# Optimization experiments

Measured on AMD Instinct MI355X. Metric: run time of the kernel, lower is better.

The kernel has to match this reference:

```python
import jax, jax.numpy as jnp
import numpy as np

B, S, P, H, W, TAG, M, K = 4, 2, 17, 128, 128, 1, 8, 10
PHW = P * H * W
SIGMA, SF = 0.2, 3.0
E_INV = float(np.e ** -1)
EPS = 1e-6


def setup_inputs() -> dict:
    key = jax.random.key(0)
    k1, k2, k3, k4, k5, k6, k7 = jax.random.split(key, 7)
    preds = jax.random.normal(k1, (B, S, (1 + TAG) * P, H, W), jnp.float32)
    gt_masks = jax.random.uniform(k2, (B, H, W), jnp.float32)
    gt_heatmaps = jax.random.uniform(k3, (B, P, H, W), jnp.float32)
    pos = jax.random.uniform(k4, (B, M, P, 2), jnp.float32) * H  # pixel coords
    vis = jax.random.randint(k5, (B, M, P, 1), 0, 2).astype(jnp.float32)
    gt_skeletons = jnp.concatenate([pos, vis], axis=-1)  # [B,M,P,3] = (x, y, vis)
    kp_idx = jax.random.randint(k6, (B, M, P, 1), 0, PHW)
    kp_vis = jax.random.randint(k7, (B, M, P, 1), 0, 2)
    gt_keypoints = jnp.concatenate([kp_idx, kp_vis], axis=-1).astype(jnp.int32)  # [B,M,J,2]
    return {"preds": preds, "gt_masks": gt_masks, "gt_heatmaps": gt_heatmaps,
            "gt_skeletons": gt_skeletons, "gt_keypoints": gt_keypoints}


def _clog(x):
    # torch BCE clamps log at -100
    return jnp.clip(jnp.log(x), -100.0, None)


def _tag_single(pt, kp):
    # pt: [TAG, PHW] tag map for one (image, stack); kp: [M, J, 2] int (flat_idx, vis)
    idx = kp[..., 0]
    vis = (kp[..., 1] > 0).astype(pt.dtype)  # [M, J]
    g = jnp.transpose(pt[:, idx], (1, 2, 0))  # [M, J, TAG]
    cnt = vis.sum(1)  # [M]
    valid = (cnt > 0).astype(pt.dtype)
    safe = jnp.maximum(cnt, 1.0)
    mean_tag = (g * vis[..., None]).sum(1) / safe[:, None]  # [M, TAG]
    # pull: per-person mean over (visible joints x tag dims) of squared deviation
    pull_pp = (((g - mean_tag[:, None]) ** 2) * vis[..., None]).sum((1, 2)) / (safe * TAG)
    num = valid.sum()
    pull = (pull_pp * valid).sum() / (num + EPS)
    d = ((mean_tag[:, None] - mean_tag[None]) ** 2).sum(-1)  # [M, M]
    pm = jnp.exp(-d) * valid[:, None] * valid[None]
    push = (pm.sum() - num) / ((num - 1.0) * num + EPS) * 0.5
    return push, pull


def _forward(preds, gt_masks, gt_heatmaps, gt_skeletons, gt_keypoints):
    hm = preds[:, :, :P]  # [B,S,P,H,W] raw heatmap logits
    prob = jax.nn.sigmoid(hm)
    # ---- detection loss (weighted BCE, per stack) ----
    t = (gt_heatmaps > E_INV).astype(jnp.float32)[:, None]  # [B,1,P,H,W]
    wgt = 10.0 * t + 0.5 * (gt_heatmaps < E_INV).astype(jnp.float32)[:, None]
    x = prob * gt_masks[:, None, None]
    bce = -(t * _clog(x) + (1.0 - t) * _clog(1.0 - x))
    det_loss = (wgt * bce).mean(axis=(0, 2, 3, 4))  # [S]
    # ---- associative embedding push/pull ----
    pred_tag_imgs = preds[:, :, P:(1 + TAG) * P].reshape(B, S, TAG, P, H, W)
    pred_tags = pred_tag_imgs.reshape(B, S, TAG, PHW)
    push, pull = jax.vmap(lambda ptb, kpb: jax.vmap(lambda pt: _tag_single(pt, kpb))(ptb))(
        pred_tags, gt_keypoints)  # each [B,S]
    # ---- keypoint sampling: top-K of flattened probability maps ----
    flat = prob.reshape(B, S, PHW)
    _, topi = jax.lax.top_k(flat, K)  # [B,S,K]
    part = topi // (H * W)
    rem = topi % (H * W)
    xi = rem // W
    yi = rem % W
    pos = jnp.stack([xi, yi], -1).astype(jnp.float32)  # [B,S,K,2]
    # ---- nearest-person matching (faithful to source, incl. vis==1 penalty) ----
    max_dist = float(H + W)
    sk_t = jnp.transpose(gt_skeletons, (0, 2, 1, 3))  # [B,P,M,3]
    pidx = jnp.broadcast_to(part.reshape(B, S * K)[:, :, None, None], (B, S * K, M, 3))
    sk_sel = jnp.take_along_axis(sk_t, pidx, axis=1).reshape(B, S, K, M, 3)
    vispen = max_dist * (sk_sel[..., 2] == 1).astype(jnp.float32)  # [B,S,K,M]
    dvec = vispen[..., None] + sk_sel[..., 1:] - pos[..., None, :]
    dist = jnp.sqrt((dvec ** 2).sum(-1) + 1e-12)
    person_ids = jnp.argmin(dist, axis=-1)  # [B,S,K]
    # ---- gather tag values at sampled locations ----
    pti = jnp.transpose(pred_tag_imgs, (0, 1, 3, 4, 5, 2))  # [B,S,P,H,W,TAG]
    bb = jnp.arange(B)[:, None, None]
    ss = jnp.arange(S)[None, :, None]
    tv = pti[bb, ss, part, xi, yi]  # [B,S,K,TAG]
    # ---- SkeletonGenerator: tag-conditioned soft-argmax ----
    aff = ((pti[:, :, None] - tv[:, :, :, None, None, None, :]) ** 2).sum(-1)  # [B,S,K,P,H,W]
    logits = SF * hm[:, :, None] - aff / (2.0 * SIGMA ** 2)
    wts = jax.nn.softmax(logits.reshape(B, S, K, P, H * W), -1).reshape(B, S, K, P, H, W)
    px = (wts * jnp.arange(H, dtype=jnp.float32)[:, None]).sum((-1, -2))  # [B,S,K,P]
    py = (wts * jnp.arange(W, dtype=jnp.float32)).sum((-1, -2))
    skel = jnp.stack([px, py], -1)  # [B,S,K,P,2]
    gts = gt_skeletons[bb, person_ids]  # [B,S,K,P,3]
    err = jnp.sqrt(((gts[..., :2] - skel) ** 2).sum(-1) + 1e-12) * (gts[..., 2] > 0)
    delta = 0.1
    a = jnp.abs(err)
    small = (a < delta).astype(jnp.float32)
    hub = small * err ** 2 + (1.0 - small) * delta * (a - delta / 2.0)
    skel_loss = hub.mean(-1).mean(-1)  # [B,S]
    # ---- weighted sum (loss_weights = (1,1,1,10)) ----
    return (1.0 * push.mean() + 1.0 * pull.mean() + 1.0 * det_loss.mean()
            + 10.0 * skel_loss.mean())


def reference(preds, gt_masks, gt_heatmaps, gt_skeletons, gt_keypoints):
    return _forward(preds, gt_masks, gt_heatmaps, gt_skeletons, gt_keypoints)
```

## Files before the change

### kernel.cpp

```cpp
#include <hip/hip_runtime.h>
#include <math.h>

#define B_ 4
#define S_ 2
#define P_ 17
#define H_ 128
#define W_ 128
#define M_ 8
#define K_ 10
#define HW_ (H_*W_)
#define PHW_ (P_*HW_)
#define CH_ 34
#define G_ 68
#define C_ 4096
#define E_INV_F 0.36787944117144233f
#define LOG2E 1.4426950408889634f
#define SF_ 3.0f
#define INV2SIG 12.5f
#define MAXDIST 256.0f

#define MAIN_BLOCKS (B_*S_*G_)
#define SKEL_CHUNKS 4
#define NBSP (B_*S_*P_)
#define SKEL_BLOCKS (NBSP*SKEL_CHUNKS)

__device__ __forceinline__ unsigned int map32(float f) {
    unsigned int u = __float_as_uint(f);
    unsigned int flip = (unsigned int)((int)u >> 31) | 0x80000000u;
    return u ^ flip;
}

__device__ __forceinline__ void insert10(unsigned long long* a, unsigned long long key) {
    bool c[10];
    #pragma unroll
    for (int j = 0; j < 10; ++j) c[j] = key > a[j];
    #pragma unroll
    for (int j = 9; j >= 1; --j)
        a[j] = c[j-1] ? a[j-1] : (c[j] ? key : a[j]);
    a[0] = c[0] ? key : a[0];
}

__device__ __forceinline__ void merge10(unsigned long long* a, const unsigned long long* b) {
    #pragma unroll
    for (int t = 0; t < 10; ++t) {
        unsigned long long key = b[t];
        if (key > a[9]) insert10(a, key);
    }
}

__global__ __launch_bounds__(256) void k_main(const float* __restrict__ preds,
                                              const float* __restrict__ gmask,
                                              const float* __restrict__ gh,
                                              unsigned long long* __restrict__ cand,
                                              float* __restrict__ ws_det) {
    int bs = blockIdx.x / G_;
    int c  = blockIdx.x % G_;
    int p    = c >> 2;
    int quarter = c & 3;
    int b    = bs / S_;
    int tid  = threadIdx.x;
    const float4* base = (const float4*)preds + (size_t)bs*CH_*4096 + (size_t)c*1024;
    const float4* gm4p = (const float4*)gmask + (size_t)b*4096 + quarter*1024;
    const float4* gh4p = (const float4*)gh + ((size_t)b*P_ + p)*4096 + quarter*1024;

    unsigned long long a[10];
    #pragma unroll
    for (int j = 0; j < 10; ++j) a[j] = 0ull;
    float det_acc = 0.0f;

    #pragma unroll
    for (int j = 0; j < 4; ++j) {
        int q = j*256 + tid;
        float4 hv = base[q];
        float4 gm = gm4p[q];
        float4 gv = gh4p[q];
        unsigned int i0 = (unsigned int)(c*C_ + q*4);
        const float* hvv = &hv.x; const float* gmv = &gm.x; const float* ghv4 = &gv.x;
        #pragma unroll
        for (int cc = 0; cc < 4; ++cc) {
            float hm = hvv[cc];
            unsigned long long key =
                ((unsigned long long)map32(hm) << 32) | (unsigned int)(~(i0 + cc));
            insert10(a, key);
            float e = exp2f(-fabsf(hm)*LOG2E);
            float r = __builtin_amdgcn_rcpf(1.0f + e);
            float prob = (hm >= 0.0f) ? r : e*r;
            float x = prob * gmv[cc];
            float ghv = ghv4[cc];
            float tt  = (ghv > E_INV_F) ? 1.0f : 0.0f;
            float wgt = 10.0f*tt + ((ghv < E_INV_F) ? 0.5f : 0.0f);
            float lx  = fmaxf(__logf(x),        -100.0f);
            float l1x = fmaxf(__logf(1.0f - x), -100.0f);
            det_acc += wgt * (-(tt*lx + (1.0f - tt)*l1x));
        }
    }
    #pragma unroll
    for (int off = 32; off > 0; off >>= 1) det_acc += __shfl_down(det_acc, off);
    __shared__ float sred[4];
    int wave = tid >> 6, lane = tid & 63;
    if (lane == 0) sred[wave] = det_acc;
    __shared__ unsigned long long sm[256*10];
    #pragma unroll
    for (int j = 0; j < 10; ++j) sm[tid*10+j] = a[j];
    __syncthreads();
    if (tid == 0) ws_det[blockIdx.x] = sred[0] + sred[1] + sred[2] + sred[3];
    for (int st = 128; st >= 1; st >>= 1) {
        if (tid < st) {
            unsigned long long x[10], y[10];
            #pragma unroll
            for (int j = 0; j < 10; ++j) { x[j] = sm[tid*10+j]; y[j] = sm[(tid+st)*10+j]; }
            merge10(x, y);
            #pragma unroll
            for (int j = 0; j < 10; ++j) sm[tid*10+j] = x[j];
        }
        __syncthreads();
    }
    if (tid < 10) cand[(size_t)blockIdx.x*10 + tid] = sm[tid];
}

__global__ __launch_bounds__(256) void k_tt(const float* __restrict__ preds,
                                            const float* __restrict__ gsk,
                                            const int* __restrict__ kp,
                                            const unsigned long long* __restrict__ cand,
                                            float* __restrict__ ws_tag,
                                            float* __restrict__ ws_tv,
                                            int* __restrict__ ws_pid) {
    int bs = blockIdx.x; int b = bs / S_;
    int tid = threadIdx.x;
    const float* tagbase = preds + ((size_t)bs*CH_ + P_)*HW_;
    __shared__ float g[M_*P_];
    __shared__ float vis[M_*P_];
    __shared__ float mean_tag[M_];
    __shared__ float validm[M_];
    __shared__ float pull_pp[M_];
    if (tid < M_*P_) {
        int m = tid / P_; int pp = tid % P_;
        int off = ((b*M_ + m)*P_ + pp)*2;
        int idx = kp[off];
        int v   = kp[off+1];
        g[tid]   = tagbase[idx];
        vis[tid] = (v > 0) ? 1.0f : 0.0f;
    }
    __syncthreads();
    if (tid < M_) {
        float cnt = 0.0f, sum = 0.0f;
        for (int pp = 0; pp < P_; pp++) { cnt += vis[tid*P_+pp]; sum += g[tid*P_+pp]*vis[tid*P_+pp]; }
        float safe = fmaxf(cnt, 1.0f);
        float mt = sum / safe;
        mean_tag[tid] = mt;
        validm[tid] = (cnt > 0.0f) ? 1.0f : 0.0f;
        float pl = 0.0f;
        for (int pp = 0; pp < P_; pp++) { float d = g[tid*P_+pp] - mt; pl += d*d*vis[tid*P_+pp]; }
        pull_pp[tid] = pl / safe;
    }
    __syncthreads();
    if (tid == 0) {
        float num = 0.0f;
        for (int m = 0; m < M_; m++) num += validm[m];
        float pull = 0.0f;
        for (int m = 0; m < M_; m++) pull += pull_pp[m]*validm[m];
        pull = pull / (num + 1e-6f);
        float pmsum = 0.0f;
        for (int i = 0; i < M_; i++)
            for (int j = 0; j < M_; j++) {
                float d = mean_tag[i] - mean_tag[j]; d = d*d;
                pmsum += expf(-d)*validm[i]*validm[j];
            }
        float push = (pmsum - num) / ((num - 1.0f)*num + 1e-6f) * 0.5f;
        ws_tag[bs] = push + pull;
    }
    __shared__ unsigned long long sm[128*10];
    if (tid < 128) {
        if (tid < G_) {
            #pragma unroll
            for (int j = 0; j < 10; ++j) sm[tid*10+j] = cand[((size_t)bs*G_ + tid)*10 + j];
        } else {
            #pragma unroll
            for (int j = 0; j < 10; ++j) sm[tid*10+j] = 0ull;
        }
    }
    __syncthreads();
    for (int st = 64; st >= 1; st >>= 1) {
        if (tid < st) {
            unsigned long long x[10], y[10];
            #pragma unroll
            for (int j = 0; j < 10; ++j) { x[j] = sm[tid*10+j]; y[j] = sm[(tid+st)*10+j]; }
            merge10(x, y);
            #pragma unroll
            for (int j = 0; j < 10; ++j) sm[tid*10+j] = x[j];
        }
        __syncthreads();
    }
    if (tid < K_) {
        unsigned long long key = sm[tid];
        unsigned int topi = (unsigned int)(~key);
        int part = topi >> 14;
        int rem  = topi & (HW_-1);
        int xi   = rem >> 7;
        int yi   = rem & (W_-1);
        float tv = tagbase[topi];
        float best = INFINITY; int pid = 0;
        for (int m = 0; m < M_; m++) {
            const float* sk = gsk + ((size_t)(b*M_ + m)*P_ + part)*3;
            float sk1 = sk[1], sk2 = sk[2];
            float vp = (sk2 == 1.0f) ? MAXDIST : 0.0f;
            float d0 = vp + sk1 - (float)xi;
            float d1 = vp + sk2 - (float)yi;
            float dist = sqrtf(d0*d0 + d1*d1 + 1e-12f);
            if (dist < best) { best = dist; pid = m; }
        }
        int o = bs*K_ + tid;
        ws_tv[o]  = tv;
        ws_pid[o] = pid;
    }
}

__global__ __launch_bounds__(256) void k_skel(const float* __restrict__ preds,
                                              const float* __restrict__ ws_tv,
                                              float* __restrict__ ws_skl,
                                              float* __restrict__ ws_ssx,
                                              float* __restrict__ ws_ssy) {
    int bid   = blockIdx.x / SKEL_CHUNKS;
    int chunk = blockIdx.x % SKEL_CHUNKS;
    int p  = bid % P_;
    int bs = bid / P_;
    const float4* hm4 = (const float4*)(preds + ((size_t)bs*CH_ + p)*HW_);
    const float4* tg4 = (const float4*)(preds + ((size_t)bs*CH_ + P_ + p)*HW_);
    float tv[K_];
    #pragma unroll
    for (int k = 0; k < K_; k++) tv[k] = ws_tv[bs*K_ + k];
    float l[K_], sx[K_], sy[K_];
    #pragma unroll
    for (int k = 0; k < K_; k++) { l[k] = 0.0f; sx[k] = 0.0f; sy[k] = 0.0f; }
    int tid = threadIdx.x;
    const float C2 = INV2SIG * LOG2E;
    #pragma unroll
    for (int j = 0; j < 4; ++j) {
        int q = chunk*1024 + j*256 + tid;
        float4 hv = hm4[q];
        float4 tg = tg4[q];
        float h  = (float)(q >> 5);
        float w0 = (float)((q*4) & (W_-1));
        const float* hvv = &hv.x; const float* tgv = &tg.x;
        #pragma unroll
        for (int cc = 0; cc < 4; ++cc) {
            float a2 = (SF_*LOG2E) * hvv[cc];
            float tgc = tgv[cc];
            float w = w0 + (float)cc;
            #pragma unroll
            for (int k = 0; k < K_; k++) {
                float d = tgc - tv[k];
                float e = exp2f(fmaf(-C2, d*d, a2));
                l[k] += e;
                sx[k] = fmaf(e, h, sx[k]);
                sy[k] = fmaf(e, w, sy[k]);
            }
        }
    }
    #pragma unroll
    for (int k = 0; k < K_; k++) {
        for (int off = 32; off > 0; off >>= 1) {
            l[k]  += __shfl_down(l[k],  off);
            sx[k] += __shfl_down(sx[k], off);
            sy[k] += __shfl_down(sy[k], off);
        }
    }
    __shared__ float red[4][K_][3];
    int wave = tid >> 6, lane = tid & 63;
    if (lane == 0) {
        #pragma unroll
        for (int k = 0; k < K_; k++) {
            red[wave][k][0] = l[k]; red[wave][k][1] = sx[k]; red[wave][k][2] = sy[k];
        }
    }
    __syncthreads();
    if (tid < K_) {
        int k = tid;
        float L  = red[0][k][0] + red[1][k][0] + red[2][k][0] + red[3][k][0];
        float SX = red[0][k][1] + red[1][k][1] + red[2][k][1] + red[3][k][1];
        float SY = red[0][k][2] + red[1][k][2] + red[2][k][2] + red[3][k][2];
        int o = blockIdx.x*K_ + k;
        ws_skl[o] = L; ws_ssx[o] = SX; ws_ssy[o] = SY;
    }
}

__global__ __launch_bounds__(256) void k_fin(const float* __restrict__ gsk,
                                             const int* __restrict__ ws_pid,
                                             const float* __restrict__ ws_skl,
                                             const float* __restrict__ ws_ssx,
                                             const float* __restrict__ ws_ssy,
                                             const float* __restrict__ ws_det,
                                             const float* __restrict__ ws_tag,
                                             float* __restrict__ out) {
    int tid = threadIdx.x;
    float acc = 0.0f;
    for (int i = tid; i < MAIN_BLOCKS; i += 256) acc += ws_det[i];
    acc *= (1.0f/(float)(B_*S_*P_*HW_));
    if (tid < B_*S_) acc += ws_tag[tid] * (1.0f/(float)(B_*S_));
    for (int idx = tid; idx < NBSP*K_; idx += 256) {
        int bid = idx / K_;
        int k   = idx % K_;
        int p  = bid % P_;
        int bs = bid / P_;
        int b  = bs / S_;
        float L = 0.0f, SX = 0.0f, SY = 0.0f;
        #pragma unroll
        for (int c = 0; c < SKEL_CHUNKS; ++c) {
            int o = (bid*SKEL_CHUNKS + c)*K_ + k;
            L += ws_skl[o]; SX += ws_ssx[o]; SY += ws_ssy[o];
        }
        float px = SX / L, py = SY / L;
        int pid = ws_pid[bs*K_ + k];
        const float* g = gsk + ((size_t)(b*M_ + pid)*P_ + p)*3;
        float d0 = g[0] - px, d1 = g[1] - py;
        float gate = (g[2] > 0.0f) ? 1.0f : 0.0f;
        float err = sqrtf(d0*d0 + d1*d1 + 1e-12f) * gate;
        float hub = (err < 0.1f) ? err*err : 0.1f*(err - 0.05f);
        acc += hub * (10.0f/(float)(B_*S_*K_*P_));
    }
    #pragma unroll
    for (int off = 32; off > 0; off >>= 1) acc += __shfl_down(acc, off);
    __shared__ float sred[4];
    int wave = tid >> 6, lane = tid & 63;
    if (lane == 0) sred[wave] = acc;
    __syncthreads();
    if (tid == 0) out[0] = sred[0] + sred[1] + sred[2] + sred[3];
}

extern "C" void kernel_launch(void* const* d_in, const int* in_sizes, int n_in,
                              void* d_out, int out_size, void* d_ws, size_t ws_size,
                              hipStream_t stream) {
    (void)in_sizes; (void)n_in; (void)out_size; (void)ws_size;
    const float* preds = (const float*)d_in[0];
    const float* gmask = (const float*)d_in[1];
    const float* gh    = (const float*)d_in[2];
    const float* gsk   = (const float*)d_in[3];
    const int*   gkp   = (const int*)d_in[4];
    float* out = (float*)d_out;
    unsigned long long* cand = (unsigned long long*)d_ws;
    float* ws_tv  = (float*)(cand + (size_t)MAIN_BLOCKS*10);
    int*   ws_pid = (int*)(ws_tv + (size_t)B_*S_*K_);
    float* ws_skl = (float*)(ws_pid + (size_t)B_*S_*K_);
    float* ws_ssx = ws_skl + (size_t)SKEL_BLOCKS*K_;
    float* ws_ssy = ws_ssx + (size_t)SKEL_BLOCKS*K_;
    float* ws_det = ws_ssy + (size_t)SKEL_BLOCKS*K_;
    float* ws_tag = ws_det + MAIN_BLOCKS;

    hipLaunchKernelGGL(k_main, dim3(MAIN_BLOCKS), dim3(256), 0, stream,
                       preds, gmask, gh, cand, ws_det);
    hipLaunchKernelGGL(k_tt,   dim3(B_*S_),       dim3(256), 0, stream,
                       preds, gsk, gkp, cand, ws_tag, ws_tv, ws_pid);
    hipLaunchKernelGGL(k_skel, dim3(SKEL_BLOCKS), dim3(256), 0, stream,
                       preds, ws_tv, ws_skl, ws_ssx, ws_ssy);
    hipLaunchKernelGGL(k_fin,  dim3(1),           dim3(256), 0, stream,
                       gsk, ws_pid, ws_skl, ws_ssx, ws_ssy, ws_det, ws_tag, out);
}
```

Measured before the change: 136.6 us.

## Fuse four kernels into one persistent kernel with atomic grid barriers

Merges the main detection/top-k pass, the tag/top-k merge, the skeleton softmax pass and the final reduction into one kernel launch of 544 blocks. Stages are ordered by atomic counters with spin-waits, and a last-block-done pattern performs the final reduction. The goal is to remove per-launch overhead and inter-kernel gaps. In exchange it relies on all blocks being co-resident to avoid deadlock, and it adds a memset launch plus spin-wait costs.

```diff
diff --git a/kernel.cpp b/kernel.cpp
--- a/kernel.cpp
+++ b/kernel.cpp
@@ -19,10 +19,9 @@
 #define INV2SIG 12.5f
 #define MAXDIST 256.0f
 
-#define MAIN_BLOCKS (B_*S_*G_)
+#define NBLK (B_*S_*G_)
 #define SKEL_CHUNKS 4
 #define NBSP (B_*S_*P_)
-#define SKEL_BLOCKS (NBSP*SKEL_CHUNKS)
 
 __device__ __forceinline__ unsigned int map32(float f) {
     unsigned int u = __float_as_uint(f);
@@ -48,283 +47,298 @@
     }
 }
 
-__global__ __launch_bounds__(256) void k_main(const float* __restrict__ preds,
-                                              const float* __restrict__ gmask,
-                                              const float* __restrict__ gh,
-                                              unsigned long long* __restrict__ cand,
-                                              float* __restrict__ ws_det) {
-    int bs = blockIdx.x / G_;
-    int c  = blockIdx.x % G_;
-    int p    = c >> 2;
-    int quarter = c & 3;
-    int b    = bs / S_;
-    int tid  = threadIdx.x;
-    const float4* base = (const float4*)preds + (size_t)bs*CH_*4096 + (size_t)c*1024;
-    const float4* gm4p = (const float4*)gmask + (size_t)b*4096 + quarter*1024;
-    const float4* gh4p = (const float4*)gh + ((size_t)b*P_ + p)*4096 + quarter*1024;
-
-    unsigned long long a[10];
-    #pragma unroll
-    for (int j = 0; j < 10; ++j) a[j] = 0ull;
-    float det_acc = 0.0f;
-
-    #pragma unroll
-    for (int j = 0; j < 4; ++j) {
-        int q = j*256 + tid;
-        float4 hv = base[q];
-        float4 gm = gm4p[q];
-        float4 gv = gh4p[q];
-        unsigned int i0 = (unsigned int)(c*C_ + q*4);
-        const float* hvv = &hv.x; const float* gmv = &gm.x; const float* ghv4 = &gv.x;
-        #pragma unroll
-        for (int cc = 0; cc < 4; ++cc) {
-            float hm = hvv[cc];
-            unsigned long long key =
-                ((unsigned long long)map32(hm) << 32) | (unsigned int)(~(i0 + cc));
-            insert10(a, key);
-            float e = exp2f(-fabsf(hm)*LOG2E);
-            float r = __builtin_amdgcn_rcpf(1.0f + e);
-            float prob = (hm >= 0.0f) ? r : e*r;
-            float x = prob * gmv[cc];
-            float ghv = ghv4[cc];
-            float tt  = (ghv > E_INV_F) ? 1.0f : 0.0f;
-            float wgt = 10.0f*tt + ((ghv < E_INV_F) ? 0.5f : 0.0f);
-            float lx  = fmaxf(__logf(x),        -100.0f);
-            float l1x = fmaxf(__logf(1.0f - x), -100.0f);
-            det_acc += wgt * (-(tt*lx + (1.0f - tt)*l1x));
-        }
-    }
-    #pragma unroll
-    for (int off = 32; off > 0; off >>= 1) det_acc += __shfl_down(det_acc, off);
+__device__ __forceinline__ void spin_until(unsigned int* p, unsigned int target) {
+    while (__hip_atomic_load(p, __ATOMIC_ACQUIRE, __HIP_MEMORY_SCOPE_AGENT) != target) {
+        __builtin_amdgcn_s_sleep(8);
+    }
+}
+
+#define BLOCK_RELEASE(CTR)  do { __syncthreads(); __threadfence(); __syncthreads(); \
+                                 if (tid == 0) atomicAdd((CTR), 1u); } while (0)
+
+__global__ __launch_bounds__(256, 3) void k_all(const float* __restrict__ preds,
+                                                const float* __restrict__ gmask,
+                                                const float* __restrict__ gh,
+                                                const float* __restrict__ gsk,
+                                                const int* __restrict__ kp,
+                                                unsigned int* __restrict__ ctr,
+                                                unsigned long long* __restrict__ cand,
+                                                float* __restrict__ ws_tv,
+                                                int* __restrict__ ws_pid,
+                                                float* __restrict__ ws_skl,
+                                                float* __restrict__ ws_ssx,
+                                                float* __restrict__ ws_ssy,
+                                                float* __restrict__ ws_det,
+                                                float* __restrict__ ws_tag,
+                                                float* __restrict__ out) {
+    int tid = threadIdx.x;
+    int blk = blockIdx.x;
+    int wave = tid >> 6, lane = tid & 63;
+
+    __shared__ unsigned long long sm[256*10];
+    __shared__ float s_g[M_*P_], s_vis[M_*P_];
+    __shared__ float s_mt[M_], s_val[M_], s_pp[M_];
     __shared__ float sred[4];
-    int wave = tid >> 6, lane = tid & 63;
-    if (lane == 0) sred[wave] = det_acc;
-    __shared__ unsigned long long sm[256*10];
-    #pragma unroll
-    for (int j = 0; j < 10; ++j) sm[tid*10+j] = a[j];
+    __shared__ float red[4][K_][3];
+    __shared__ int   s_last;
+
+    {
+        int bs = blk / G_;
+        int c  = blk % G_;
+        int p       = c >> 2;
+        int quarter = c & 3;
+        int b       = bs / S_;
+        const float4* base = (const float4*)preds + (size_t)bs*CH_*1024*4 + (size_t)c*1024;
+        const float4* gm4p = (const float4*)gmask + (size_t)b*4096 + quarter*1024;
+        const float4* gh4p = (const float4*)gh + ((size_t)b*P_ + p)*4096 + quarter*1024;
+
+        unsigned long long a[10];
+        #pragma unroll
+        for (int j = 0; j < 10; ++j) a[j] = 0ull;
+        float det_acc = 0.0f;
+
+        #pragma unroll
+        for (int j = 0; j < 4; ++j) {
+            int q = j*256 + tid;
+            float4 hv = base[q];
+            float4 gm = gm4p[q];
+            float4 gv = gh4p[q];
+            unsigned int i0 = (unsigned int)(c*C_ + q*4);
+            const float* hvv = &hv.x; const float* gmv = &gm.x; const float* ghv4 = &gv.x;
+            #pragma unroll
+            for (int cc = 0; cc < 4; ++cc) {
+                float hm = hvv[cc];
+                unsigned long long key =
+                    ((unsigned long long)map32(hm) << 32) | (unsigned int)(~(i0 + cc));
+                insert10(a, key);
+                float e = exp2f(-fabsf(hm)*LOG2E);
+                float r = __builtin_amdgcn_rcpf(1.0f + e);
+                float prob = (hm >= 0.0f) ? r : e*r;
+                float x = prob * gmv[cc];
+                float ghv = ghv4[cc];
+                float tt  = (ghv > E_INV_F) ? 1.0f : 0.0f;
+                float wgt = 10.0f*tt + ((ghv < E_INV_F) ? 0.5f : 0.0f);
+                float lx  = fmaxf(__logf(x),        -100.0f);
+                float l1x = fmaxf(__logf(1.0f - x), -100.0f);
+                det_acc += wgt * (-(tt*lx + (1.0f - tt)*l1x));
+            }
+        }
+        #pragma unroll
+        for (int off = 32; off > 0; off >>= 1) det_acc += __shfl_down(det_acc, off);
+        if (lane == 0) sred[wave] = det_acc;
+        #pragma unroll
+        for (int j = 0; j < 10; ++j) sm[tid*10+j] = a[j];
+        __syncthreads();
+        if (tid == 0) ws_det[blk] = sred[0] + sred[1] + sred[2] + sred[3];
+        for (int st = 128; st >= 1; st >>= 1) {
+            if (tid < st) {
+                unsigned long long x[10], y[10];
+                #pragma unroll
+                for (int j = 0; j < 10; ++j) { x[j] = sm[tid*10+j]; y[j] = sm[(tid+st)*10+j]; }
+                merge10(x, y);
+                #pragma unroll
+                for (int j = 0; j < 10; ++j) sm[tid*10+j] = x[j];
+            }
+            __syncthreads();
+        }
+        if (tid < 10) cand[(size_t)blk*10 + tid] = sm[tid];
+    }
+    if (blk < B_*S_) {
+        int bs2 = blk; int b2 = bs2 / S_;
+        const float* tagbase = preds + ((size_t)bs2*CH_ + P_)*HW_;
+        if (tid < M_*P_) {
+            int m = tid / P_; int pp = tid % P_;
+            int off = ((b2*M_ + m)*P_ + pp)*2;
+            s_g[tid]   = tagbase[kp[off]];
+            s_vis[tid] = (kp[off+1] > 0) ? 1.0f : 0.0f;
+        }
+        __syncthreads();
+        if (tid < M_) {
+            float cnt = 0.0f, sum = 0.0f;
+            for (int pp = 0; pp < P_; pp++) { cnt += s_vis[tid*P_+pp]; sum += s_g[tid*P_+pp]*s_vis[tid*P_+pp]; }
+            float safe = fmaxf(cnt, 1.0f);
+            float mt = sum / safe;
+            s_mt[tid] = mt;
+            s_val[tid] = (cnt > 0.0f) ? 1.0f : 0.0f;
+            float pl = 0.0f;
+            for (int pp = 0; pp < P_; pp++) { float d = s_g[tid*P_+pp] - mt; pl += d*d*s_vis[tid*P_+pp]; }
+            s_pp[tid] = pl / safe;
+        }
+        __syncthreads();
+        if (tid == 0) {
+            float num = 0.0f;
+            for (int m = 0; m < M_; m++) num += s_val[m];
+            float pull = 0.0f;
+            for (int m = 0; m < M_; m++) pull += s_pp[m]*s_val[m];
+            pull = pull / (num + 1e-6f);
+            float pmsum = 0.0f;
+            for (int i = 0; i < M_; i++)
+                for (int j = 0; j < M_; j++) {
+                    float d = s_mt[i] - s_mt[j]; d = d*d;
+                    pmsum += expf(-d)*s_val[i]*s_val[j];
+                }
+            float push = (pmsum - num) / ((num - 1.0f)*num + 1e-6f) * 0.5f;
+            ws_tag[bs2] = push + pull;
+        }
+    }
+    BLOCK_RELEASE(&ctr[0]);
+
+    if (blk < B_*S_) {
+        if (tid == 0) spin_until(&ctr[0], NBLK);
+        __syncthreads();
+        __threadfence();
+        int bs2 = blk; int b2 = bs2 / S_;
+        if (tid < 128) {
+            if (tid < G_) {
+                #pragma unroll
+                for (int j = 0; j < 10; ++j) sm[tid*10+j] = cand[((size_t)bs2*G_ + tid)*10 + j];
+            } else {
+                #pragma unroll
+                for (int j = 0; j < 10; ++j) sm[tid*10+j] = 0ull;
+            }
+        }
+        __syncthreads();
+        for (int st = 64; st >= 1; st >>= 1) {
+            if (tid < st) {
+                unsigned long long x[10], y[10];
+                #pragma unroll
+                for (int j = 0; j < 10; ++j) { x[j] = sm[tid*10+j]; y[j] = sm[(tid+st)*10+j]; }
+                merge10(x, y);
+                #pragma unroll
+                for (int j = 0; j < 10; ++j) sm[tid*10+j] = x[j];
+            }
+            __syncthreads();
+        }
+        if (tid < K_) {
+            unsigned long long key = sm[tid];
+            unsigned int topi = (unsigned int)(~key);
+            int part = topi >> 14;
+            int rem  = topi & (HW_-1);
+            int xi   = rem >> 7;
+            int yi   = rem & (W_-1);
+            const float* tagbase = preds + ((size_t)bs2*CH_ + P_)*HW_;
+            float tv = tagbase[topi];
+            float best = INFINITY; int pid = 0;
+            for (int m = 0; m < M_; m++) {
+                const float* sk = gsk + ((size_t)(b2*M_ + m)*P_ + part)*3;
+                float sk1 = sk[1], sk2 = sk[2];
+                float vp = (sk2 == 1.0f) ? MAXDIST : 0.0f;
+                float d0 = vp + sk1 - (float)xi;
+                float d1 = vp + sk2 - (float)yi;
+                float dist = sqrtf(d0*d0 + d1*d1 + 1e-12f);
+                if (dist < best) { best = dist; pid = m; }
+            }
+            ws_tv[bs2*K_ + tid]  = tv;
+            ws_pid[bs2*K_ + tid] = pid;
+        }
+        BLOCK_RELEASE(&ctr[8]);
+    }
+    if (tid == 0) spin_until(&ctr[8], (unsigned int)(B_*S_));
     __syncthreads();
-    if (tid == 0) ws_det[blockIdx.x] = sred[0] + sred[1] + sred[2] + sred[3];
-    for (int st = 128; st >= 1; st >>= 1) {
-        if (tid < st) {
-            unsigned long long x[10], y[10];
+    __threadfence();
+
+    {
+        int bid   = blk / SKEL_CHUNKS;
+        int chunk = blk % SKEL_CHUNKS;
+        int p  = bid % P_;
+        int bs = bid / P_;
+        const float4* hm4 = (const float4*)(preds + ((size_t)bs*CH_ + p)*HW_);
+        const float4* tg4 = (const float4*)(preds + ((size_t)bs*CH_ + P_ + p)*HW_);
+        float tv[K_];
+        #pragma unroll
+        for (int k = 0; k < K_; k++) tv[k] = ws_tv[bs*K_ + k];
+        float l[K_], sx[K_], sy[K_];
+        #pragma unroll
+        for (int k = 0; k < K_; k++) { l[k] = 0.0f; sx[k] = 0.0f; sy[k] = 0.0f; }
+        const float C2 = INV2SIG * LOG2E;
+        #pragma unroll
+        for (int j = 0; j < 4; ++j) {
+            int q = chunk*1024 + j*256 + tid;
+            float4 hv = hm4[q];
+            float4 tg = tg4[q];
+            float h  = (float)(q >> 5);
+            float w0 = (float)((q*4) & (W_-1));
+            const float* hvv = &hv.x; const float* tgv = &tg.x;
             #pragma unroll
-            for (int j = 0; j < 10; ++j) { x[j] = sm[tid*10+j]; y[j] = sm[(tid+st)*10+j]; }
-            merge10(x, y);
+            for (int cc = 0; cc < 4; ++cc) {
+                float a2 = (SF_*LOG2E) * hvv[cc];
+                float tgc = tgv[cc];
+                float w = w0 + (float)cc;
+                #pragma unroll
+                for (int k = 0; k < K_; k++) {
+                    float d = tgc - tv[k];
+                    float e = exp2f(fmaf(-C2, d*d, a2));
+                    l[k] += e;
+                    sx[k] = fmaf(e, h, sx[k]);
+                    sy[k] = fmaf(e, w, sy[k]);
+                }
+            }
+        }
+        #pragma unroll
+        for (int k = 0; k < K_; k++) {
+            for (int off = 32; off > 0; off >>= 1) {
+                l[k]  += __shfl_down(l[k],  off);
+                sx[k] += __shfl_down(sx[k], off);
+                sy[k] += __shfl_down(sy[k], off);
+            }
+        }
+        if (lane == 0) {
             #pragma unroll
-            for (int j = 0; j < 10; ++j) sm[tid*10+j] = x[j];
-        }
-        __syncthreads();
-    }
-    if (tid < 10) cand[(size_t)blockIdx.x*10 + tid] = sm[tid];
-}
-
-__global__ __launch_bounds__(256) void k_tt(const float* __restrict__ preds,
-                                            const float* __restrict__ gsk,
-                                            const int* __restrict__ kp,
-                                            const unsigned long long* __restrict__ cand,
-                                            float* __restrict__ ws_tag,
-                                            float* __restrict__ ws_tv,
-                                            int* __restrict__ ws_pid) {
-    int bs = blockIdx.x; int b = bs / S_;
-    int tid = threadIdx.x;
-    const float* tagbase = preds + ((size_t)bs*CH_ + P_)*HW_;
-    __shared__ float g[M_*P_];
-    __shared__ float vis[M_*P_];
-    __shared__ float mean_tag[M_];
-    __shared__ float validm[M_];
-    __shared__ float pull_pp[M_];
-    if (tid < M_*P_) {
-        int m = tid / P_; int pp = tid % P_;
-        int off = ((b*M_ + m)*P_ + pp)*2;
-        int idx = kp[off];
-        int v   = kp[off+1];
-        g[tid]   = tagbase[idx];
-        vis[tid] = (v > 0) ? 1.0f : 0.0f;
+            for (int k = 0; k < K_; k++) {
+                red[wave][k][0] = l[k]; red[wave][k][1] = sx[k]; red[wave][k][2] = sy[k];
+            }
+        }
+        __syncthreads();
+        if (tid < K_) {
+            int k = tid;
+            float L  = red[0][k][0] + red[1][k][0] + red[2][k][0] + red[3][k][0];
+            float SX = red[0][k][1] + red[1][k][1] + red[2][k][1] + red[3][k][1];
+            float SY = red[0][k][2] + red[1][k][2] + red[2][k][2] + red[3][k][2];
+            int o = blk*K_ + k;
+            ws_skl[o] = L; ws_ssx[o] = SX; ws_ssy[o] = SY;
+        }
     }
     __syncthreads();
-    if (tid < M_) {
-        float cnt = 0.0f, sum = 0.0f;
-        for (int pp = 0; pp < P_; pp++) { cnt += vis[tid*P_+pp]; sum += g[tid*P_+pp]*vis[tid*P_+pp]; }
-        float safe = fmaxf(cnt, 1.0f);
-        float mt = sum / safe;
-        mean_tag[tid] = mt;
-        validm[tid] = (cnt > 0.0f) ? 1.0f : 0.0f;
-        float pl = 0.0f;
-        for (int pp = 0; pp < P_; pp++) { float d = g[tid*P_+pp] - mt; pl += d*d*vis[tid*P_+pp]; }
-        pull_pp[tid] = pl / safe;
-    }
+    __threadfence();
     __syncthreads();
     if (tid == 0) {
-        float num = 0.0f;
-        for (int m = 0; m < M_; m++) num += validm[m];
-        float pull = 0.0f;
-        for (int m = 0; m < M_; m++) pull += pull_pp[m]*validm[m];
-        pull = pull / (num + 1e-6f);
-        float pmsum = 0.0f;
-        for (int i = 0; i < M_; i++)
-            for (int j = 0; j < M_; j++) {
-                float d = mean_tag[i] - mean_tag[j]; d = d*d;
-                pmsum += expf(-d)*validm[i]*validm[j];
-            }
-        float push = (pmsum - num) / ((num - 1.0f)*num + 1e-6f) * 0.5f;
-        ws_tag[bs] = push + pull;
-    }
-    __shared__ unsigned long long sm[128*10];
-    if (tid < 128) {
-        if (tid < G_) {
+        unsigned int old = atomicAdd(&ctr[16], 1u);
+        s_last = (old == NBLK - 1) ? 1 : 0;
+    }
+    __syncthreads();
+    if (s_last) {
+        __threadfence();
+        float acc = 0.0f;
+        for (int i = tid; i < NBLK; i += 256) acc += ws_det[i];
+        acc *= (1.0f/(float)(B_*S_*P_*HW_));
+        if (tid < B_*S_) acc += ws_tag[tid] * (1.0f/(float)(B_*S_));
+        for (int idx = tid; idx < NBSP*K_; idx += 256) {
+            int bid = idx / K_;
+            int k   = idx % K_;
+            int p  = bid % P_;
+            int bs = bid / P_;
+            int b  = bs / S_;
+            float L = 0.0f, SX = 0.0f, SY = 0.0f;
             #pragma unroll
-            for (int j = 0; j < 10; ++j) sm[tid*10+j] = cand[((size_t)bs*G_ + tid)*10 + j];
-        } else {
-            #pragma unroll
-            for (int j = 0; j < 10; ++j) sm[tid*10+j] = 0ull;
-        }
-    }
-    __syncthreads();
-    for (int st = 64; st >= 1; st >>= 1) {
-        if (tid < st) {
-            unsigned long long x[10], y[10];
-            #pragma unroll
-            for (int j = 0; j < 10; ++j) { x[j] = sm[tid*10+j]; y[j] = sm[(tid+st)*10+j]; }
-            merge10(x, y);
-            #pragma unroll
-            for (int j = 0; j < 10; ++j) sm[tid*10+j] = x[j];
-        }
-        __syncthreads();
-    }
-    if (tid < K_) {
-        unsigned long long key = sm[tid];
-        unsigned int topi = (unsigned int)(~key);
-        int part = topi >> 14;
-        int rem  = topi & (HW_-1);
-        int xi   = rem >> 7;
-        int yi   = rem & (W_-1);
-        float tv = tagbase[topi];
-        float best = INFINITY; int pid = 0;
-        for (int m = 0; m < M_; m++) {
-            const float* sk = gsk + ((size_t)(b*M_ + m)*P_ + part)*3;
-            float sk1 = sk[1], sk2 = sk[2];
-            float vp = (sk2 == 1.0f) ? MAXDIST : 0.0f;
-            float d0 = vp + sk1 - (float)xi;
-            float d1 = vp + sk2 - (float)yi;
-            float dist = sqrtf(d0*d0 + d1*d1 + 1e-12f);
-            if (dist < best) { best = dist; pid = m; }
-        }
-        int o = bs*K_ + tid;
-        ws_tv[o]  = tv;
-        ws_pid[o] = pid;
-    }
-}
-
-__global__ __launch_bounds__(256) void k_skel(const float* __restrict__ preds,
-                                              const float* __restrict__ ws_tv,
-                                              float* __restrict__ ws_skl,
-                                              float* __restrict__ ws_ssx,
-                                              float* __restrict__ ws_ssy) {
-    int bid   = blockIdx.x / SKEL_CHUNKS;
-    int chunk = blockIdx.x % SKEL_CHUNKS;
-    int p  = bid % P_;
-    int bs = bid / P_;
-    const float4* hm4 = (const float4*)(preds + ((size_t)bs*CH_ + p)*HW_);
-    const float4* tg4 = (const float4*)(preds + ((size_t)bs*CH_ + P_ + p)*HW_);
-    float tv[K_];
-    #pragma unroll
-    for (int k = 0; k < K_; k++) tv[k] = ws_tv[bs*K_ + k];
-    float l[K_], sx[K_], sy[K_];
-    #pragma unroll
-    for (int k = 0; k < K_; k++) { l[k] = 0.0f; sx[k] = 0.0f; sy[k] = 0.0f; }
-    int tid = threadIdx.x;
-    const float C2 = INV2SIG * LOG2E;
-    #pragma unroll
-    for (int j = 0; j < 4; ++j) {
-        int q = chunk*1024 + j*256 + tid;
-        float4 hv = hm4[q];
-        float4 tg = tg4[q];
-        float h  = (float)(q >> 5);
-        float w0 = (float)((q*4) & (W_-1));
-        const float* hvv = &hv.x; const float* tgv = &tg.x;
-        #pragma unroll
-        for (int cc = 0; cc < 4; ++cc) {
-            float a2 = (SF_*LOG2E) * hvv[cc];
-            float tgc = tgv[cc];
-            float w = w0 + (float)cc;
-            #pragma unroll
-            for (int k = 0; k < K_; k++) {
-                float d = tgc - tv[k];
-                float e = exp2f(fmaf(-C2, d*d, a2));
-                l[k] += e;
-                sx[k] = fmaf(e, h, sx[k]);
-                sy[k] = fmaf(e, w, sy[k]);
-            }
-        }
-    }
-    #pragma unroll
-    for (int k = 0; k < K_; k++) {
-        for (int off = 32; off > 0; off >>= 1) {
-            l[k]  += __shfl_down(l[k],  off);
-            sx[k] += __shfl_down(sx[k], off);
-            sy[k] += __shfl_down(sy[k], off);
-        }
-    }
-    __shared__ float red[4][K_][3];
-    int wave = tid >> 6, lane = tid & 63;
-    if (lane == 0) {
-        #pragma unroll
-        for (int k = 0; k < K_; k++) {
-            red[wave][k][0] = l[k]; red[wave][k][1] = sx[k]; red[wave][k][2] = sy[k];
-        }
-    }
-    __syncthreads();
-    if (tid < K_) {
-        int k = tid;
-        float L  = red[0][k][0] + red[1][k][0] + red[2][k][0] + red[3][k][0];
-        float SX = red[0][k][1] + red[1][k][1] + red[2][k][1] + red[3][k][1];
-        float SY = red[0][k][2] + red[1][k][2] + red[2][k][2] + red[3][k][2];
-        int o = blockIdx.x*K_ + k;
-        ws_skl[o] = L; ws_ssx[o] = SX; ws_ssy[o] = SY;
-    }
-}
-
-__global__ __launch_bounds__(256) void k_fin(const float* __restrict__ gsk,
-                                             const int* __restrict__ ws_pid,
-                                             const float* __restrict__ ws_skl,
-                                             const float* __restrict__ ws_ssx,
-                                             const float* __restrict__ ws_ssy,
-                                             const float* __restrict__ ws_det,
-                                             const float* __restrict__ ws_tag,
-                                             float* __restrict__ out) {
-    int tid = threadIdx.x;
-    float acc = 0.0f;
-    for (int i = tid; i < MAIN_BLOCKS; i += 256) acc += ws_det[i];
-    acc *= (1.0f/(float)(B_*S_*P_*HW_));
-    if (tid < B_*S_) acc += ws_tag[tid] * (1.0f/(float)(B_*S_));
-    for (int idx = tid; idx < NBSP*K_; idx += 256) {
-        int bid = idx / K_;
-        int k   = idx % K_;
-        int p  = bid % P_;
-        int bs = bid / P_;
-        int b  = bs / S_;
-        float L = 0.0f, SX = 0.0f, SY = 0.0f;
-        #pragma unroll
-        for (int c = 0; c < SKEL_CHUNKS; ++c) {
-            int o = (bid*SKEL_CHUNKS + c)*K_ + k;
-            L += ws_skl[o]; SX += ws_ssx[o]; SY += ws_ssy[o];
-        }
-        float px = SX / L, py = SY / L;
-        int pid = ws_pid[bs*K_ + k];
-        const float* g = gsk + ((size_t)(b*M_ + pid)*P_ + p)*3;
-        float d0 = g[0] - px, d1 = g[1] - py;
-        float gate = (g[2] > 0.0f) ? 1.0f : 0.0f;
-        float err = sqrtf(d0*d0 + d1*d1 + 1e-12f) * gate;
-        float hub = (err < 0.1f) ? err*err : 0.1f*(err - 0.05f);
-        acc += hub * (10.0f/(float)(B_*S_*K_*P_));
-    }
-    #pragma unroll
-    for (int off = 32; off > 0; off >>= 1) acc += __shfl_down(acc, off);
-    __shared__ float sred[4];
-    int wave = tid >> 6, lane = tid & 63;
-    if (lane == 0) sred[wave] = acc;
-    __syncthreads();
-    if (tid == 0) out[0] = sred[0] + sred[1] + sred[2] + sred[3];
+            for (int c = 0; c < SKEL_CHUNKS; ++c) {
+                int o = (bid*SKEL_CHUNKS + c)*K_ + k;
+                L += ws_skl[o]; SX += ws_ssx[o]; SY += ws_ssy[o];
+            }
+            float px = SX / L, py = SY / L;
+            int pid = ws_pid[bs*K_ + k];
+            const float* g = gsk + ((size_t)(b*M_ + pid)*P_ + p)*3;
+            float d0 = g[0] - px, d1 = g[1] - py;
+            float gate = (g[2] > 0.0f) ? 1.0f : 0.0f;
+            float err = sqrtf(d0*d0 + d1*d1 + 1e-12f) * gate;
+            float hub = (err < 0.1f) ? err*err : 0.1f*(err - 0.05f);
+            acc += hub * (10.0f/(float)(B_*S_*K_*P_));
+        }
+        #pragma unroll
+        for (int off = 32; off > 0; off >>= 1) acc += __shfl_down(acc, off);
+        if (lane == 0) sred[wave] = acc;
+        __syncthreads();
+        if (tid == 0) out[0] = sred[0] + sred[1] + sred[2] + sred[3];
+    }
 }
 
 extern "C" void kernel_launch(void* const* d_in, const int* in_sizes, int n_in,
@@ -337,21 +351,20 @@
     const float* gsk   = (const float*)d_in[3];
     const int*   gkp   = (const int*)d_in[4];
     float* out = (float*)d_out;
-    unsigned long long* cand = (unsigned long long*)d_ws;
-    float* ws_tv  = (float*)(cand + (size_t)MAIN_BLOCKS*10);
+
+    unsigned int* ctr = (unsigned int*)d_ws;
+    char* base = (char*)d_ws + 256;
+    unsigned long long* cand = (unsigned long long*)base;
+    float* ws_tv  = (float*)(cand + (size_t)NBLK*10);
     int*   ws_pid = (int*)(ws_tv + (size_t)B_*S_*K_);
     float* ws_skl = (float*)(ws_pid + (size_t)B_*S_*K_);
-    float* ws_ssx = ws_skl + (size_t)SKEL_BLOCKS*K_;
-    float* ws_ssy = ws_ssx + (size_t)SKEL_BLOCKS*K_;
-    float* ws_det = ws_ssy + (size_t)SKEL_BLOCKS*K_;
-    float* ws_tag = ws_det + MAIN_BLOCKS;
-
-    hipLaunchKernelGGL(k_main, dim3(MAIN_BLOCKS), dim3(256), 0, stream,
-                       preds, gmask, gh, cand, ws_det);
-    hipLaunchKernelGGL(k_tt,   dim3(B_*S_),       dim3(256), 0, stream,
-                       preds, gsk, gkp, cand, ws_tag, ws_tv, ws_pid);
-    hipLaunchKernelGGL(k_skel, dim3(SKEL_BLOCKS), dim3(256), 0, stream,
-                       preds, ws_tv, ws_skl, ws_ssx, ws_ssy);
-    hipLaunchKernelGGL(k_fin,  dim3(1),           dim3(256), 0, stream,
-                       gsk, ws_pid, ws_skl, ws_ssx, ws_ssy, ws_det, ws_tag, out);
-}
+    float* ws_ssx = ws_skl + (size_t)NBLK*K_;
+    float* ws_ssy = ws_ssx + (size_t)NBLK*K_;
+    float* ws_det = ws_ssy + (size_t)NBLK*K_;
+    float* ws_tag = ws_det + NBLK;
+
+    hipMemsetAsync(d_ws, 0, 256, stream);
+    hipLaunchKernelGGL(k_all, dim3(NBLK), dim3(256), 0, stream,
+                       preds, gmask, gh, gsk, gkp, ctr, cand,
+                       ws_tv, ws_pid, ws_skl, ws_ssx, ws_ssy, ws_det, ws_tag, out);
+}
```

After: 325.6 us. 138% more time.
